# Optimization experiments

Measured on AMD Instinct MI355X. Metric: run time of the kernel, lower is better.

The kernel has to match this reference:

```python
import jax, jax.numpy as jnp
import numpy as np

N_PTS = 50000   # number of mesh points (n)
K_PTS = 16      # kernel points per kernel (k)
N_KER = 64      # number of learnable kernels
SIGMA = 1.0


def setup_inputs() -> dict:
    key = jax.random.key(0)
    k1, k2, k3 = jax.random.split(key, 3)
    normal = jax.random.normal(k1, (N_PTS * 3,), dtype=jnp.float32)
    neighbour = jax.random.randint(k2, (N_PTS * 3,), 0, N_PTS, dtype=jnp.int32)
    kernel = jax.random.normal(k3, (N_KER, K_PTS, 3), dtype=jnp.float32)
    return {"normal": normal, "neighbour": neighbour, "kernel": kernel}


def reference(normal, neighbour, kernel):
    n = normal.shape[0] // 3
    pts = normal.reshape(n, 3)                 # [n,3] per-point normals
    nbr = neighbour.reshape(n, 3)              # [n,3] neighbor indices a,b,c
    # gather self + 3 neighbors -> [n,4,3]
    idx = jnp.concatenate([jnp.arange(n, dtype=nbr.dtype)[:, None], nbr], axis=1)
    g = pts[idx]                               # [n,4,3]
    # squared distance ||g - kernel||^2 via expansion (avoids [n,4,64,k,3])
    g2 = jnp.sum(g * g, axis=-1)[:, :, None, None]      # [n,4,1,1]
    k2 = jnp.sum(kernel * kernel, axis=-1)               # [64,k]
    cross = jnp.einsum('npd,mld->npml', g, kernel)       # [n,4,64,k]
    d2 = g2 + k2[None, None, :, :] - 2.0 * cross         # [n,4,64,k]
    corr = jnp.exp(-d2) / (2.0 * SIGMA * SIGMA)
    out = corr.sum(axis=(1, 3)) / (K_PTS * 4)            # [n,64]
    return out.reshape(-1)                               # [n*64]
```

## Files before the change

kernel.cpp:

```cpp
#include <hip/hip_runtime.h>

#define N_KER 64
#define K_PTS 16
#define LOG2E 1.44269504088896340736f

__global__ __launch_bounds__(256, 8) void corr_kernel(
    const float* __restrict__ normal,
    const int*   __restrict__ neighbour,
    const float* __restrict__ kern,
    float*       __restrict__ out,
    int n)
{
    __shared__ float4 ksp[K_PTS * N_KER];

    const int tid = threadIdx.x;

    #pragma unroll
    for (int it = 0; it < 4; ++it) {
        int j = it * 256 + tid;
        int m = j & 63;
        int l = j >> 6;
        const float* kp = kern + (m * K_PTS + l) * 3;
        float x = kp[0], y = kp[1], z = kp[2];
        ksp[l * N_KER + m] = make_float4(2.0f * LOG2E * x,
                                         2.0f * LOG2E * y,
                                         2.0f * LOG2E * z,
                                         -LOG2E * (x * x + y * y + z * z));
    }
    __syncthreads();

    const int wave = tid >> 6;
    const int m    = tid & 63;
    const int i    = blockIdx.x * 4 + wave;
    if (i >= n) return;

    const int ia = neighbour[i * 3 + 0];
    const int ib = neighbour[i * 3 + 1];
    const int ic = neighbour[i * 3 + 2];
    int idxs[4] = { i, ia, ib, ic };

    float gx[4], gy[4], gz[4], ea[4], acc[4];
    #pragma unroll
    for (int p = 0; p < 4; ++p) {
        int q = idxs[p];
        float x = normal[q * 3 + 0];
        float y = normal[q * 3 + 1];
        float z = normal[q * 3 + 2];
        gx[p] = x; gy[p] = y; gz[p] = z;
        ea[p] = __builtin_amdgcn_exp2f(-LOG2E * (x * x + y * y + z * z));
        acc[p] = 0.0f;
    }

    #pragma unroll 4
    for (int l = 0; l < K_PTS; ++l) {
        float4 k4 = ksp[l * N_KER + m];
        #pragma unroll
        for (int p = 0; p < 4; ++p)
            acc[p] += __builtin_amdgcn_exp2f(
                fmaf(gx[p], k4.x, fmaf(gy[p], k4.y, fmaf(gz[p], k4.z, k4.w))));
    }

    float s = ea[0] * acc[0] + ea[1] * acc[1] + ea[2] * acc[2] + ea[3] * acc[3];
    out[(size_t)i * N_KER + m] = s * (1.0f / 128.0f);
}

extern "C" void kernel_launch(void* const* d_in, const int* in_sizes, int n_in,
                              void* d_out, int out_size, void* d_ws, size_t ws_size,
                              hipStream_t stream) {
    const float* normal    = (const float*)d_in[0];
    const int*   neighbour = (const int*)d_in[1];
    const float* kern      = (const float*)d_in[2];
    float*       out       = (float*)d_out;

    int n = in_sizes[0] / 3;
    int blocks = (n + 3) / 4;
    corr_kernel<<<blocks, 256, 0, stream>>>(normal, neighbour, kern, out, n);
}
```

Measured before the change: 97.03 us.

## Split into per-point precompute and neighbour-gather sum via workspace

Each point's per-kernel exp sum is now computed once in a first kernel and stored in a workspace buffer. A second kernel sums the self and three neighbour rows with float2 loads and scales the result. This removes the 4x redundant exp work, since every point was previously recomputed as a neighbour of others. In exchange it adds a second launch plus about 12.8MB of workspace writes and random row gathers. The old fused kernel is kept as a fallback when the workspace is too small.

```diff
diff --git a/kernel.cpp b/kernel.cpp
--- a/kernel.cpp
+++ b/kernel.cpp
@@ -4,17 +4,16 @@
 #define K_PTS 16
 #define LOG2E 1.44269504088896340736f
 
-__global__ __launch_bounds__(256, 8) void corr_kernel(
+
+__global__ __launch_bounds__(256, 8) void corr_phase1(
     const float* __restrict__ normal,
-    const int*   __restrict__ neighbour,
     const float* __restrict__ kern,
-    float*       __restrict__ out,
+    float*       __restrict__ S,
     int n)
 {
     __shared__ float4 ksp[K_PTS * N_KER];
 
     const int tid = threadIdx.x;
-
     #pragma unroll
     for (int it = 0; it < 4; ++it) {
         int j = it * 256 + tid;
@@ -31,14 +30,82 @@
 
     const int wave = tid >> 6;
     const int m    = tid & 63;
+    const int q0   = blockIdx.x * 8 + wave * 2;
+    const int qa   = min(q0,     n - 1);
+    const int qb   = min(q0 + 1, n - 1);
+
+    float ax = normal[qa * 3 + 0], ay = normal[qa * 3 + 1], az = normal[qa * 3 + 2];
+    float bx = normal[qb * 3 + 0], by = normal[qb * 3 + 1], bz = normal[qb * 3 + 2];
+    float ea = __builtin_amdgcn_exp2f(-LOG2E * (ax * ax + ay * ay + az * az));
+    float eb = __builtin_amdgcn_exp2f(-LOG2E * (bx * bx + by * by + bz * bz));
+
+    float acc0 = 0.0f, acc1 = 0.0f;
+    #pragma unroll 4
+    for (int l = 0; l < K_PTS; ++l) {
+        float4 k4 = ksp[l * N_KER + m];
+        acc0 += __builtin_amdgcn_exp2f(
+            fmaf(ax, k4.x, fmaf(ay, k4.y, fmaf(az, k4.z, k4.w))));
+        acc1 += __builtin_amdgcn_exp2f(
+            fmaf(bx, k4.x, fmaf(by, k4.y, fmaf(bz, k4.z, k4.w))));
+    }
+
+    if (q0     < n) S[(size_t)q0       * N_KER + m] = ea * acc0;
+    if (q0 + 1 < n) S[(size_t)(q0 + 1) * N_KER + m] = eb * acc1;
+}
+
+__global__ __launch_bounds__(256) void corr_phase2(
+    const float2* __restrict__ S2,
+    const int*    __restrict__ neighbour,
+    float2*       __restrict__ out2,
+    int n)
+{
+    int t = blockIdx.x * 256 + threadIdx.x;
+    int total2 = n * (N_KER / 2);
+    if (t >= total2) return;
+    int i  = t >> 5;
+    int h  = t & 31;
+    int a = neighbour[i * 3 + 0];
+    int b = neighbour[i * 3 + 1];
+    int c = neighbour[i * 3 + 2];
+    float2 s0 = S2[t];
+    float2 s1 = S2[(size_t)a * 32 + h];
+    float2 s2 = S2[(size_t)b * 32 + h];
+    float2 s3 = S2[(size_t)c * 32 + h];
+    float2 r;
+    r.x = (s0.x + s1.x + s2.x + s3.x) * (1.0f / 128.0f);
+    r.y = (s0.y + s1.y + s2.y + s3.y) * (1.0f / 128.0f);
+    out2[t] = r;
+}
+
+__global__ __launch_bounds__(256, 8) void corr_fused(
+    const float* __restrict__ normal,
+    const int*   __restrict__ neighbour,
+    const float* __restrict__ kern,
+    float*       __restrict__ out,
+    int n)
+{
+    __shared__ float4 ksp[K_PTS * N_KER];
+    const int tid = threadIdx.x;
+    #pragma unroll
+    for (int it = 0; it < 4; ++it) {
+        int j = it * 256 + tid;
+        int m = j & 63;
+        int l = j >> 6;
+        const float* kp = kern + (m * K_PTS + l) * 3;
+        float x = kp[0], y = kp[1], z = kp[2];
+        ksp[l * N_KER + m] = make_float4(2.0f * LOG2E * x, 2.0f * LOG2E * y,
+                                         2.0f * LOG2E * z,
+                                         -LOG2E * (x * x + y * y + z * z));
+    }
+    __syncthreads();
+    const int wave = tid >> 6;
+    const int m    = tid & 63;
     const int i    = blockIdx.x * 4 + wave;
     if (i >= n) return;
-
     const int ia = neighbour[i * 3 + 0];
     const int ib = neighbour[i * 3 + 1];
     const int ic = neighbour[i * 3 + 2];
     int idxs[4] = { i, ia, ib, ic };
-
     float gx[4], gy[4], gz[4], ea[4], acc[4];
     #pragma unroll
     for (int p = 0; p < 4; ++p) {
@@ -50,7 +117,6 @@
         ea[p] = __builtin_amdgcn_exp2f(-LOG2E * (x * x + y * y + z * z));
         acc[p] = 0.0f;
     }
-
     #pragma unroll 4
     for (int l = 0; l < K_PTS; ++l) {
         float4 k4 = ksp[l * N_KER + m];
@@ -59,7 +125,6 @@
             acc[p] += __builtin_amdgcn_exp2f(
                 fmaf(gx[p], k4.x, fmaf(gy[p], k4.y, fmaf(gz[p], k4.z, k4.w))));
     }
-
     float s = ea[0] * acc[0] + ea[1] * acc[1] + ea[2] * acc[2] + ea[3] * acc[3];
     out[(size_t)i * N_KER + m] = s * (1.0f / 128.0f);
 }
@@ -73,6 +138,18 @@
     float*       out       = (float*)d_out;
 
     int n = in_sizes[0] / 3;
-    int blocks = (n + 3) / 4;
-    corr_kernel<<<blocks, 256, 0, stream>>>(normal, neighbour, kern, out, n);
+    size_t need = (size_t)n * N_KER * sizeof(float);
+
+    if (ws_size >= need) {
+        float* S = (float*)d_ws;
+        int blocks1 = (n + 7) / 8;
+        corr_phase1<<<blocks1, 256, 0, stream>>>(normal, kern, S, n);
+        int total2  = n * (N_KER / 2);
+        int blocks2 = (total2 + 255) / 256;
+        corr_phase2<<<blocks2, 256, 0, stream>>>((const float2*)S, neighbour,
+                                                 (float2*)out, n);
+    } else {
+        int blocks = (n + 3) / 4;
+        corr_fused<<<blocks, 256, 0, stream>>>(normal, neighbour, kern, out, n);
+    }
 }
```

Measured after the change: 88.09 us. 9.2% less time.
